# Kernel tuning notes

Measured on AMD Instinct MI355X. Metric: run time of the kernel, lower is better.

Reference implementation:

```python
import jax, jax.numpy as jnp
import numpy as np

IN_CHANNELS = 192
KERNEL_SIZE = 3
GROUPS = 1
N_ITER = 3  # power_it_niter


def _gram_conv(K):
    """Gram step of the conv operator: G[a, b] = sum_o corr(K[o, a], K[o, b]).

    K: (co, ci, k, k) -> (ci, ci, 2k-1, 2k-1). This is the kernel of M^T M
    where M is the (zero-padded) conv operator with kernel K.
    """
    k = K.shape[-1]
    lhs = jnp.transpose(K, (1, 0, 2, 3))  # batch = a-index, channels = o
    rhs = jnp.transpose(K, (1, 0, 2, 3))  # out-chan = b-index, in-chan = o
    return jax.lax.conv_general_dilated(
        lhs, rhs, window_strides=(1, 1),
        padding=[(k - 1, k - 1), (k - 1, k - 1)],
        dimension_numbers=("NCHW", "OIHW", "NCHW"))


def _sigma_one_group(K, n_iter):
    """Gram-iteration spectral-norm estimate (Delattre et al. 2024).

    sigma(K_0) ~= prod_t f_t^(1/2^t) * ||K_T||_F^(1/2^T), f_t = Frobenius norm
    before each Gram squaring (normalization keeps values in fp range).
    """
    log_sigma = jnp.asarray(0.0, K.dtype)
    for t in range(n_iter):  # static unroll: kernel spatial size grows k -> 2k-1
        f = jnp.sqrt(jnp.sum(K * K))
        K = K / f
        log_sigma = log_sigma + jnp.log(f) / (2.0 ** t)
        K = _gram_conv(K)
    f_final = jnp.sqrt(jnp.sum(K * K))
    log_sigma = log_sigma + jnp.log(f_final) / (2.0 ** n_iter)
    return jnp.exp(log_sigma)


def compute_delattre2024(K, n_iter):
    # K: (groups, c, c, k, k) -> (groups,) per-group spectral norm estimates
    return jax.vmap(lambda g: _sigma_one_group(g, n_iter))(K)


def setup_inputs() -> dict:
    key = jax.random.key(0)
    kernel = jax.random.normal(
        key, (IN_CHANNELS * GROUPS, IN_CHANNELS, KERNEL_SIZE, KERNEL_SIZE),
        dtype=jnp.float32)
    return {"kernel": kernel}


def reference(kernel):
    g = GROUPS
    c = IN_CHANNELS // GROUPS
    K = kernel.reshape(g, c, c, KERNEL_SIZE, KERNEL_SIZE)
    sigmas = compute_delattre2024(K, N_ITER)  # (groups,)
    K = K / sigmas.reshape(-1, 1, 1, 1, 1)
    return K.reshape(IN_CHANNELS * GROUPS, IN_CHANNELS, KERNEL_SIZE, KERNEL_SIZE)
```

## Files before the change

kernel.cpp:

```cpp
#include <hip/hip_runtime.h>
#include <hip/hip_bf16.h>

typedef __bf16 bf16;
typedef __attribute__((ext_vector_type(8))) __bf16 bf16x8;
typedef __attribute__((ext_vector_type(4))) float f32x4;
typedef __attribute__((ext_vector_type(4))) int i32x4;

#define CH 192
#define MAT (CH * CH)
#define NF 145
#define FSTRIDE (2 * MAT)
#define NELEM (CH * CH * 9)
#define XSCALE 9.765625e-4f
#define W17 0.36959913571644626f


__global__ void k_dft(const float* __restrict__ K, bf16* __restrict__ X,
                      float* __restrict__ s3) {
    __shared__ float twc[17], tws[17];
    int bid = blockIdx.x;
    int xcd = bid & 7;
    int r = bid >> 3;
    int g4 = r / 144, sub = r % 144;
    int t = threadIdx.x;
    if (bid == 0 && t == 0) *s3 = 0.0f;
    if (t < 17) {
        float s, c;
        __sincosf(-W17 * (float)t, &s, &c);
        twc[t] = c; tws[t] = s;
    }
    int p = sub * 256 + t;
    int a = p / CH, o = p % CH;
    const float* src = K + (size_t)(o * CH + a) * 9;
    float kv[9];
#pragma unroll
    for (int i = 0; i < 9; ++i) kv[i] = src[i];
    __syncthreads();
#pragma unroll
    for (int jj = 0; jj < 4; ++jj) {
        int f = xcd + 8 * (g4 * 4 + jj);
        if (f >= NF) break;
        int fy, fx;
        if (f < 9) { fy = 0; fx = f; }
        else { int u = f - 9; fy = 1 + u / 17; fx = u % 17; }
        float pyr = twc[fy], pyi = tws[fy];
        float pxr = twc[fx], pxi = tws[fx];
        int fx2 = 2 * fx; if (fx2 >= 17) fx2 -= 17;
        int fy2 = 2 * fy; if (fy2 >= 17) fy2 -= 17;
        float px2r = twc[fx2], px2i = tws[fx2];
        float py2r = twc[fy2], py2i = tws[fy2];
        float s0r = kv[0] + kv[1] * pxr + kv[2] * px2r, s0i = kv[1] * pxi + kv[2] * px2i;
        float s1r = kv[3] + kv[4] * pxr + kv[5] * px2r, s1i = kv[4] * pxi + kv[5] * px2i;
        float s2r = kv[6] + kv[7] * pxr + kv[8] * px2r, s2i = kv[7] * pxi + kv[8] * px2i;
        float ar = s0r + pyr * s1r - pyi * s1i + py2r * s2r - py2i * s2i;
        float ai = s0i + pyr * s1i + pyi * s1r + py2r * s2i + py2i * s2r;
        size_t base = (size_t)f * FSTRIDE;
        X[base + p]       = (bf16)(ar * XSCALE);
        X[base + MAT + p] = (bf16)(ai * XSCALE);
    }
}

#define LDSR 72
#define SLAB (96 * LDSR)
#define OLDSR 104

template <bool WRITE, bool NORM>
__global__ __launch_bounds__(256, 2) void k_gram(const bf16* __restrict__ X,
                                                 bf16* __restrict__ Y,
                                                 float* __restrict__ s3) {
    __shared__ bf16 lds[4 * SLAB];
    __shared__ float red[4];
    int bid = blockIdx.x;
    int xcd = bid & 7, r = bid >> 3;
    int fi = r / 3, q = r % 3;
    int f = xcd + 8 * fi;
    if (f >= NF) return;
    int row0 = (q == 2) ? 96 : 0;
    int col0 = (q >= 1) ? 96 : 0;
    bool diag = (q != 1);
    int sb = diag ? 0 : 2;
    const bf16* Xf = X + (size_t)f * FSTRIDE;

    int tid = threadIdx.x;
    int lane = tid & 63, w = tid >> 6;
    int wr = (w >> 1) * 48, wc = (w & 1) * 48;
    int ml = lane & 15, kq = (lane >> 4) * 8;

    f32x4 cr[3][3], ci[3][3];
#pragma unroll
    for (int i = 0; i < 3; ++i)
#pragma unroll
        for (int j = 0; j < 3; ++j) {
            cr[i][j] = f32x4{0.f, 0.f, 0.f, 0.f};
            ci[i][j] = f32x4{0.f, 0.f, 0.f, 0.f};
        }

    for (int kc = 0; kc < CH; kc += 64) {
        i32x4 v[12];
#pragma unroll
        for (int s = 0; s < 2; ++s) {
            const bf16* src = Xf + (s ? MAT : 0) + (size_t)row0 * CH + kc;
#pragma unroll
            for (int j = 0; j < 3; ++j) {
                int chunk = j * 256 + tid;
                int rr = chunk >> 3, c8 = chunk & 7;
                v[s * 3 + j] = *(const i32x4*)(src + rr * CH + c8 * 8);
            }
        }
        if (!diag) {
#pragma unroll
            for (int s = 2; s < 4; ++s) {
                const bf16* src = Xf + ((s & 1) ? MAT : 0) + (size_t)col0 * CH + kc;
#pragma unroll
                for (int j = 0; j < 3; ++j) {
                    int chunk = j * 256 + tid;
                    int rr = chunk >> 3, c8 = chunk & 7;
                    v[s * 3 + j] = *(const i32x4*)(src + rr * CH + c8 * 8);
                }
            }
        }
        __syncthreads();
#pragma unroll
        for (int s = 0; s < 2; ++s)
#pragma unroll
            for (int j = 0; j < 3; ++j) {
                int chunk = j * 256 + tid;
                int rr = chunk >> 3, c8 = chunk & 7;
                *(i32x4*)&lds[s * SLAB + rr * LDSR + c8 * 8] = v[s * 3 + j];
            }
        if (!diag) {
#pragma unroll
            for (int s = 2; s < 4; ++s)
#pragma unroll
                for (int j = 0; j < 3; ++j) {
                    int chunk = j * 256 + tid;
                    int rr = chunk >> 3, c8 = chunk & 7;
                    *(i32x4*)&lds[s * SLAB + rr * LDSR + c8 * 8] = v[s * 3 + j];
                }
        }
        __syncthreads();

#pragma unroll
        for (int ks = 0; ks < 64; ks += 32) {
            bf16x8 ar[3], ai[3], nai[3], br[3], bi[3];
            int ko = ks + kq;
#pragma unroll
            for (int mt = 0; mt < 3; ++mt) {
                ar[mt] = *(const bf16x8*)&lds[0 * SLAB + (wr + mt * 16 + ml) * LDSR + ko];
                ai[mt] = *(const bf16x8*)&lds[1 * SLAB + (wr + mt * 16 + ml) * LDSR + ko];
                br[mt] = *(const bf16x8*)&lds[(sb + 0) * SLAB + (wc + mt * 16 + ml) * LDSR + ko];
                bi[mt] = *(const bf16x8*)&lds[(sb + 1) * SLAB + (wc + mt * 16 + ml) * LDSR + ko];
                i32x4 u = __builtin_bit_cast(i32x4, ai[mt]);
                u ^= 0x80008000;
                nai[mt] = __builtin_bit_cast(bf16x8, u);
            }
#pragma unroll
            for (int mt = 0; mt < 3; ++mt)
#pragma unroll
                for (int nt = 0; nt < 3; ++nt) {
                    cr[mt][nt] = __builtin_amdgcn_mfma_f32_16x16x32_bf16(ar[mt],  br[nt], cr[mt][nt], 0, 0, 0);
                    cr[mt][nt] = __builtin_amdgcn_mfma_f32_16x16x32_bf16(ai[mt],  bi[nt], cr[mt][nt], 0, 0, 0);
                    ci[mt][nt] = __builtin_amdgcn_mfma_f32_16x16x32_bf16(ar[mt],  bi[nt], ci[mt][nt], 0, 0, 0);
                    ci[mt][nt] = __builtin_amdgcn_mfma_f32_16x16x32_bf16(nai[mt], br[nt], ci[mt][nt], 0, 0, 0);
                }
        }
    }

    if (WRITE) {
        bf16* tileA = lds;
        bf16* tileB = lds + 96 * OLDSR;
        bf16* Yf = Y + (size_t)f * FSTRIDE;
        int lr0 = wr + (lane >> 4) * 4;
        int lc0 = wc + ml;
#pragma unroll
        for (int part = 0; part < 2; ++part) {
            __syncthreads();
#pragma unroll
            for (int mt = 0; mt < 3; ++mt)
#pragma unroll
                for (int nt = 0; nt < 3; ++nt)
#pragma unroll
                    for (int rr = 0; rr < 4; ++rr) {
                        float vv = part ? ci[mt][nt][rr] : cr[mt][nt][rr];
                        int rrow = lr0 + mt * 16 + rr;
                        int ccol = lc0 + nt * 16;
                        tileA[rrow * OLDSR + ccol] = (bf16)vv;
                        if (q == 1)
                            tileB[ccol * OLDSR + rrow] = (bf16)(part ? -vv : vv);
                    }
            __syncthreads();
            bf16* dst = Yf + (part ? MAT : 0) + (size_t)row0 * CH + col0;
            for (int ch = tid; ch < 96 * 12; ch += 256) {
                int rw = ch / 12, cc = ch % 12;
                *(i32x4*)&dst[(size_t)rw * CH + cc * 8] = *(const i32x4*)&tileA[rw * OLDSR + cc * 8];
            }
            if (q == 1) {
                bf16* dst2 = Yf + (part ? MAT : 0) + (size_t)col0 * CH + row0;
                for (int ch = tid; ch < 96 * 12; ch += 256) {
                    int rw = ch / 12, cc = ch % 12;
                    *(i32x4*)&dst2[(size_t)rw * CH + cc * 8] = *(const i32x4*)&tileB[rw * OLDSR + cc * 8];
                }
            }
        }
    }
    if (NORM) {
        float loc = 0.f;
#pragma unroll
        for (int mt = 0; mt < 3; ++mt)
#pragma unroll
            for (int nt = 0; nt < 3; ++nt)
#pragma unroll
                for (int rr = 0; rr < 4; ++rr)
                    loc += cr[mt][nt][rr] * cr[mt][nt][rr] + ci[mt][nt][rr] * ci[mt][nt][rr];
#pragma unroll
        for (int off = 32; off > 0; off >>= 1) loc += __shfl_down(loc, off, 64);
        if (lane == 0) red[w] = loc;
        __syncthreads();
        if (tid == 0) {
            float base = (f == 0) ? 1.0f : 2.0f;
            float wq = (q == 1) ? 2.0f : 1.0f;
            atomicAdd(s3, base * wq * (red[0] + red[1] + red[2] + red[3]));
        }
    }
}

__global__ void k_scale(const float* __restrict__ K, float* __restrict__ out,
                        const float* __restrict__ s3) {
    float sig = 1024.0f * exp2f(log2f((*s3) * (1.0f / 289.0f)) * 0.0625f);
    float inv = 1.0f / sig;
    int i = (blockIdx.x * 256 + threadIdx.x) * 4;
    f32x4 v = *(const f32x4*)(K + i);
    v *= inv;
    *(f32x4*)(out + i) = v;
}

extern "C" void kernel_launch(void* const* d_in, const int* in_sizes, int n_in,
                              void* d_out, int out_size, void* d_ws, size_t ws_size,
                              hipStream_t stream) {
    const float* K = (const float*)d_in[0];
    float* out = (float*)d_out;
    char* ws = (char*)d_ws;
    float* s3 = (float*)ws;
    bf16* bufX = (bf16*)(ws + 256);
    bf16* bufH = bufX + (size_t)NF * FSTRIDE;

    k_dft<<<8 * 5 * 144, 256, 0, stream>>>(K, bufX, s3);
    k_gram<true,  false><<<8 * 19 * 3, 256, 0, stream>>>(bufX, bufH, nullptr);
    k_gram<true,  false><<<8 * 19 * 3, 256, 0, stream>>>(bufH, bufX, nullptr);
    k_gram<false, true ><<<8 * 19 * 3, 256, 0, stream>>>(bufX, nullptr, s3);
    k_scale<<<NELEM / 1024, 256, 0, stream>>>(K, out, s3);
}
```

Baseline: 109.4 us.

## Compute DFT via split-bf16 MFMA and fuse final scaling into last Gram kernel

Replaces the per-element scalar DFT kernel with a matrix-multiply formulation: kernel taps and twiddle factors are split into bf16 hi/lo parts and multiplied with three MFMAs to keep near-fp32 accuracy, using 288 blocks instead of 5760. It also removes the separate scale kernel. Extra blocks appended to the last Gram launch spin on an atomic counter until all active Gram blocks have added their norm contributions, then scale the output. This saves a launch and shortens the DFT, but the spin-wait relies on the Gram blocks being scheduled before or alongside the waiting blocks.

```diff
diff --git a/kernel.cpp b/kernel.cpp
--- a/kernel.cpp
+++ b/kernel.cpp
@@ -5,6 +5,7 @@
 typedef __attribute__((ext_vector_type(8))) __bf16 bf16x8;
 typedef __attribute__((ext_vector_type(4))) float f32x4;
 typedef __attribute__((ext_vector_type(4))) int i32x4;
+typedef __attribute__((ext_vector_type(2))) int i32x2;
 
 #define CH 192
 #define MAT (CH * CH)
@@ -13,50 +14,84 @@
 #define NELEM (CH * CH * 9)
 #define XSCALE 9.765625e-4f
 #define W17 0.36959913571644626f
-
-
-__global__ void k_dft(const float* __restrict__ K, bf16* __restrict__ X,
-                      float* __restrict__ s3) {
+#define NGRAM (8 * 19 * 3)
+#define NACT 435
+#define NSCALE 324
+
+
+#define TSTR 40
+__global__ __launch_bounds__(256) void k_dftm(const float* __restrict__ K,
+                                              bf16* __restrict__ X,
+                                              float* __restrict__ s3,
+                                              int* __restrict__ cnt) {
+    __shared__ bf16 Th[304 * TSTR], Tl[304 * TSTR];
     __shared__ float twc[17], tws[17];
-    int bid = blockIdx.x;
-    int xcd = bid & 7;
-    int r = bid >> 3;
-    int g4 = r / 144, sub = r % 144;
-    int t = threadIdx.x;
-    if (bid == 0 && t == 0) *s3 = 0.0f;
-    if (t < 17) {
+    int tid = threadIdx.x;
+    if (blockIdx.x == 0 && tid == 0) { *s3 = 0.0f; *cnt = 0; }
+    if (tid < 17) {
         float s, c;
-        __sincosf(-W17 * (float)t, &s, &c);
-        twc[t] = c; tws[t] = s;
-    }
-    int p = sub * 256 + t;
-    int a = p / CH, o = p % CH;
-    const float* src = K + (size_t)(o * CH + a) * 9;
-    float kv[9];
-#pragma unroll
-    for (int i = 0; i < 9; ++i) kv[i] = src[i];
+        __sincosf(-W17 * (float)tid, &s, &c);
+        twc[tid] = c; tws[tid] = s;
+    }
+    for (int i = tid; i < 304 * TSTR / 4; i += 256) {
+        ((i32x2*)Th)[i] = i32x2{0, 0};
+        ((i32x2*)Tl)[i] = i32x2{0, 0};
+    }
     __syncthreads();
-#pragma unroll
-    for (int jj = 0; jj < 4; ++jj) {
-        int f = xcd + 8 * (g4 * 4 + jj);
-        if (f >= NF) break;
+    for (int pr = tid; pr < NF * 9; pr += 256) {
+        int f = pr / 9, k = pr % 9;
         int fy, fx;
         if (f < 9) { fy = 0; fx = f; }
         else { int u = f - 9; fy = 1 + u / 17; fx = u % 17; }
-        float pyr = twc[fy], pyi = tws[fy];
-        float pxr = twc[fx], pxi = tws[fx];
-        int fx2 = 2 * fx; if (fx2 >= 17) fx2 -= 17;
-        int fy2 = 2 * fy; if (fy2 >= 17) fy2 -= 17;
-        float px2r = twc[fx2], px2i = tws[fx2];
-        float py2r = twc[fy2], py2i = tws[fy2];
-        float s0r = kv[0] + kv[1] * pxr + kv[2] * px2r, s0i = kv[1] * pxi + kv[2] * px2i;
-        float s1r = kv[3] + kv[4] * pxr + kv[5] * px2r, s1i = kv[4] * pxi + kv[5] * px2i;
-        float s2r = kv[6] + kv[7] * pxr + kv[8] * px2r, s2i = kv[7] * pxi + kv[8] * px2i;
-        float ar = s0r + pyr * s1r - pyi * s1i + py2r * s2r - py2i * s2i;
-        float ai = s0i + pyr * s1i + pyi * s1r + py2r * s2i + py2i * s2r;
-        size_t base = (size_t)f * FSTRIDE;
-        X[base + p]       = (bf16)(ar * XSCALE);
-        X[base + MAT + p] = (bf16)(ai * XSCALE);
+        int ph = (fy * (k / 3) + fx * (k % 3)) % 17;
+        float vr = twc[ph] * XSCALE, vi = tws[ph] * XSCALE;
+        bf16 hr = (bf16)vr, hi = (bf16)vi;
+        Th[(2 * f) * TSTR + k] = hr;  Tl[(2 * f) * TSTR + k] = (bf16)(vr - (float)hr);
+        Th[(2 * f + 1) * TSTR + k] = hi;  Tl[(2 * f + 1) * TSTR + k] = (bf16)(vi - (float)hi);
+    }
+    __syncthreads();
+
+    int lane = tid & 63, w = tid >> 6;
+    int ml = lane & 15, kq4 = lane >> 4;
+    int Pb0 = blockIdx.x * 128;
+    bf16x8 Ah[2], Al[2];
+#pragma unroll
+    for (int pt = 0; pt < 2; ++pt) {
+        int p = Pb0 + (w * 2 + pt) * 16 + ml;
+        int a = p / CH, o = p % CH;
+        const float* src = K + (size_t)(o * CH + a) * 9;
+        bf16x8 h8, l8;
+#pragma unroll
+        for (int jj = 0; jj < 8; ++jj) {
+            int k = kq4 * 8 + jj;
+            float kv = (k < 9) ? src[k] : 0.0f;
+            bf16 h = (bf16)kv;
+            h8[jj] = h;
+            l8[jj] = (bf16)(kv - (float)h);
+        }
+        Ah[pt] = h8; Al[pt] = l8;
+    }
+#pragma unroll 4
+    for (int ct = 0; ct < 19; ++ct) {
+        int c = ct * 16 + ml;
+        bf16x8 Bh = *(const bf16x8*)&Th[c * TSTR + kq4 * 8];
+        bf16x8 Bl = *(const bf16x8*)&Tl[c * TSTR + kq4 * 8];
+#pragma unroll
+        for (int pt = 0; pt < 2; ++pt) {
+            f32x4 acc = f32x4{0.f, 0.f, 0.f, 0.f};
+            acc = __builtin_amdgcn_mfma_f32_16x16x32_bf16(Al[pt], Bh, acc, 0, 0, 0);
+            acc = __builtin_amdgcn_mfma_f32_16x16x32_bf16(Ah[pt], Bl, acc, 0, 0, 0);
+            acc = __builtin_amdgcn_mfma_f32_16x16x32_bf16(Ah[pt], Bh, acc, 0, 0, 0);
+            if (c < 2 * NF) {
+                int f = c >> 1, part = c & 1;
+                int p0 = Pb0 + (w * 2 + pt) * 16 + kq4 * 4;
+                bf16* dst = X + (size_t)f * FSTRIDE + part * MAT + p0;
+                alignas(8) bf16 tmp[4];
+#pragma unroll
+                for (int r = 0; r < 4; ++r) tmp[r] = (bf16)acc[r];
+                *(i32x2*)dst = *(const i32x2*)tmp;
+            }
+        }
     }
 }
 
@@ -67,10 +102,32 @@
 template <bool WRITE, bool NORM>
 __global__ __launch_bounds__(256, 2) void k_gram(const bf16* __restrict__ X,
                                                  bf16* __restrict__ Y,
-                                                 float* __restrict__ s3) {
+                                                 float* __restrict__ s3,
+                                                 int* __restrict__ cnt,
+                                                 const float* __restrict__ Kin,
+                                                 float* __restrict__ outp) {
     __shared__ bf16 lds[4 * SLAB];
     __shared__ float red[4];
     int bid = blockIdx.x;
+    int tid = threadIdx.x;
+
+    if (NORM && bid >= NGRAM) {
+        int sb = bid - NGRAM;
+        if (tid == 0) {
+            while (__hip_atomic_load(cnt, __ATOMIC_ACQUIRE, __HIP_MEMORY_SCOPE_AGENT) < NACT)
+                __builtin_amdgcn_s_sleep(32);
+        }
+        __syncthreads();
+        float sv = __hip_atomic_load(s3, __ATOMIC_RELAXED, __HIP_MEMORY_SCOPE_AGENT);
+        float sig = 1024.0f * exp2f(log2f(sv * (1.0f / 289.0f)) * 0.0625f);
+        float inv = 1.0f / sig;
+        int i = (sb * 256 + tid) * 4;
+        f32x4 v = *(const f32x4*)(Kin + i);
+        v *= inv;
+        *(f32x4*)(outp + i) = v;
+        return;
+    }
+
     int xcd = bid & 7, r = bid >> 3;
     int fi = r / 3, q = r % 3;
     int f = xcd + 8 * fi;
@@ -78,10 +135,9 @@
     int row0 = (q == 2) ? 96 : 0;
     int col0 = (q >= 1) ? 96 : 0;
     bool diag = (q != 1);
-    int sb = diag ? 0 : 2;
+    int sb2 = diag ? 0 : 2;
     const bf16* Xf = X + (size_t)f * FSTRIDE;
 
-    int tid = threadIdx.x;
     int lane = tid & 63, w = tid >> 6;
     int wr = (w >> 1) * 48, wc = (w & 1) * 48;
     int ml = lane & 15, kq = (lane >> 4) * 8;
@@ -148,8 +204,8 @@
             for (int mt = 0; mt < 3; ++mt) {
                 ar[mt] = *(const bf16x8*)&lds[0 * SLAB + (wr + mt * 16 + ml) * LDSR + ko];
                 ai[mt] = *(const bf16x8*)&lds[1 * SLAB + (wr + mt * 16 + ml) * LDSR + ko];
-                br[mt] = *(const bf16x8*)&lds[(sb + 0) * SLAB + (wc + mt * 16 + ml) * LDSR + ko];
-                bi[mt] = *(const bf16x8*)&lds[(sb + 1) * SLAB + (wc + mt * 16 + ml) * LDSR + ko];
+                br[mt] = *(const bf16x8*)&lds[(sb2 + 0) * SLAB + (wc + mt * 16 + ml) * LDSR + ko];
+                bi[mt] = *(const bf16x8*)&lds[(sb2 + 1) * SLAB + (wc + mt * 16 + ml) * LDSR + ko];
                 i32x4 u = __builtin_bit_cast(i32x4, ai[mt]);
                 u ^= 0x80008000;
                 nai[mt] = __builtin_bit_cast(bf16x8, u);
@@ -220,18 +276,10 @@
             float base = (f == 0) ? 1.0f : 2.0f;
             float wq = (q == 1) ? 2.0f : 1.0f;
             atomicAdd(s3, base * wq * (red[0] + red[1] + red[2] + red[3]));
-        }
-    }
-}
-
-__global__ void k_scale(const float* __restrict__ K, float* __restrict__ out,
-                        const float* __restrict__ s3) {
-    float sig = 1024.0f * exp2f(log2f((*s3) * (1.0f / 289.0f)) * 0.0625f);
-    float inv = 1.0f / sig;
-    int i = (blockIdx.x * 256 + threadIdx.x) * 4;
-    f32x4 v = *(const f32x4*)(K + i);
-    v *= inv;
-    *(f32x4*)(out + i) = v;
+            __threadfence();
+            atomicAdd(cnt, 1);
+        }
+    }
 }
 
 extern "C" void kernel_launch(void* const* d_in, const int* in_sizes, int n_in,
@@ -241,12 +289,12 @@
     float* out = (float*)d_out;
     char* ws = (char*)d_ws;
     float* s3 = (float*)ws;
+    int* cnt = (int*)(ws + 4);
     bf16* bufX = (bf16*)(ws + 256);
     bf16* bufH = bufX + (size_t)NF * FSTRIDE;
 
-    k_dft<<<8 * 5 * 144, 256, 0, stream>>>(K, bufX, s3);
-    k_gram<true,  false><<<8 * 19 * 3, 256, 0, stream>>>(bufX, bufH, nullptr);
-    k_gram<true,  false><<<8 * 19 * 3, 256, 0, stream>>>(bufH, bufX, nullptr);
-    k_gram<false, true ><<<8 * 19 * 3, 256, 0, stream>>>(bufX, nullptr, s3);
-    k_scale<<<NELEM / 1024, 256, 0, stream>>>(K, out, s3);
+    k_dftm<<<288, 256, 0, stream>>>(K, bufX, s3, cnt);
+    k_gram<true,  false><<<NGRAM, 256, 0, stream>>>(bufX, bufH, nullptr, nullptr, nullptr, nullptr);
+    k_gram<true,  false><<<NGRAM, 256, 0, stream>>>(bufH, bufX, nullptr, nullptr, nullptr, nullptr);
+    k_gram<false, true ><<<NGRAM + NSCALE, 256, 0, stream>>>(bufX, nullptr, s3, cnt, K, out);
 }
```

Measured after the change: 150.0 us. +37.1%, slower.
